# Performance work log

Measured on AMD Instinct MI355X. Metric: run time of the kernel, lower is better.

Reference implementation:

```python
import jax, jax.numpy as jnp
import numpy as np

A_MAX = 7  # 2**A_bits - 1 with A_bits=3
W_HI = 7   # torch.randint(0, 2**W_bits - 1) -> values in [0, 6]


def _conv_valid(x, w):
    # x: [N,C,H,W] float32, w: [O,I,kh,kw] float32; stride 1, no padding
    return jax.lax.conv_general_dilated(
        x, w, window_strides=(1, 1), padding='VALID',
        dimension_numbers=('NCHW', 'OIHW', 'NCHW'))


def setup_inputs() -> dict:
    key = jax.random.key(0)
    k_x, k_w = jax.random.split(key)
    x = jax.random.randint(k_x, (16, 64, 112, 112), 0, 8, dtype=jnp.int32)
    # 3-bit weights of the original 7x7 conv, values 0..6
    W7 = jax.random.randint(k_w, (128, 64, 7, 7), 0, W_HI).astype(jnp.float32)
    w1 = W7[:, :, :, 0:3]
    w2 = W7[:, :, :, 2:5]
    w2 = w2.at[:, :, :, 0].set(0.0)
    w2 = w2.at[:, :, :, 2].set(0.0)
    w3 = W7[:, :, :, 4:7]
    return {"x": x, "w1": w1, "w2": w2, "w3": w3}


def reference(x, w1, w2, w3):
    # 3-bit activation quantization: clip int input to [0, 7]
    xc = jnp.clip(x, 0, A_MAX).astype(jnp.float32)
    out1 = _conv_valid(xc[:, :, :, :-2], w1)   # [N,O,H-6,W-4]
    out2 = _conv_valid(xc, w2)                 # [N,O,H-6,W-2]
    out3 = _conv_valid(xc[:, :, :, 2:], w3)    # [N,O,H-6,W-4]
    # combine slices -> equivalent to valid 7x7 conv: [N,O,H-6,W-6]
    return out1[:, :, :, :-2] + out2[:, :, :, 2:-2] + out3[:, :, :, 2:]
```

## Files before the change

### kernel.cpp

```cpp
#include <hip/hip_runtime.h>
#include <cstdint>

typedef __attribute__((ext_vector_type(4))) int i32x4;

#define XROWS  22
#define ROWB   2048
#define WSLICE 8192
#define WB_BYTES 409600
#define XT_BYTES ((size_t)16 * 112 * 128 * 64)
#define GRID_MAIN 1536

__device__ __forceinline__ void g2lds16(const void* g, void* l) {
  __builtin_amdgcn_global_load_lds(
      (const __attribute__((address_space(1))) unsigned int*)g,
      (__attribute__((address_space(3))) unsigned int*)l, 16, 0, 0);
}

__global__ void prep_w(const float* __restrict__ w1,
                       const float* __restrict__ w2,
                       const float* __restrict__ w3,
                       signed char* __restrict__ wb) {
  int t = blockIdx.x * 256 + threadIdx.x;
  int lo = t & 15;
  int co = (t >> 4) & 127;
  int g  = (t >> 11) & 3;
  int s  = t >> 13;
  if (s >= 49) return;
  int kh = s / 7, kw = s % 7;
  int ci = g * 16 + lo;
  int base = ((co * 64 + ci) * 7 + kh) * 3;
  float v;
  if (kw < 3)       v = w1[base + kw];
  else if (kw == 3) v = w2[base + 1];
  else              v = w3[base + kw - 4];
  wb[t] = (signed char)(int)v;
}

__global__ void prep_xw(const int* __restrict__ x,
                        const float* __restrict__ w1,
                        const float* __restrict__ w2,
                        const float* __restrict__ w3,
                        signed char* __restrict__ xt,
                        signed char* __restrict__ wb) {
  __shared__ unsigned char T[64 * 68];
  const int tid = threadIdx.x;
  const int wt = blockIdx.x * 64, h = blockIdx.y, n = blockIdx.z;
  const int fid = (blockIdx.z * 112 + blockIdx.y) * 2 + blockIdx.x;

  if (fid < 1568) {
    int t = fid * 256 + tid;
    int lo = t & 15;
    int co = (t >> 4) & 127;
    int g  = (t >> 11) & 3;
    int s  = t >> 13;
    int kh = s / 7, kw = s % 7;
    int ci = g * 16 + lo;
    int base = ((co * 64 + ci) * 7 + kh) * 3;
    float v;
    if (kw < 3)       v = w1[base + kw];
    else if (kw == 3) v = w2[base + 1];
    else              v = w3[base + kw - 4];
    wb[t] = (signed char)(int)v;
  }

  {
    const int wr = tid & 63;
    const int cb = (tid >> 6) * 16;
    int ws = wt + wr; ws = ws < 112 ? ws : 111;
    const int* xp = x + (((size_t)n * 64 + cb) * 112 + h) * 112 + ws;
    #pragma unroll
    for (int g4 = 0; g4 < 4; ++g4) {
      uint32_t v = 0;
      #pragma unroll
      for (int j = 0; j < 4; ++j) {
        int a = xp[(g4 * 4 + j) * 12544];
        a = a < 0 ? 0 : (a > 7 ? 7 : a);
        v |= (uint32_t)a << (8 * j);
      }
      *(uint32_t*)&T[wr * 68 + cb + g4 * 4] = v;
    }
  }
  __syncthreads();
  {
    const int wo = tid >> 2, q = tid & 3;
    const int key = ((wt + wo) >> 1) & 3;
    const int sg = (q ^ key) << 4;
    int4 v;
    v.x = *(const int*)&T[wo * 68 + sg + 0];
    v.y = *(const int*)&T[wo * 68 + sg + 4];
    v.z = *(const int*)&T[wo * 68 + sg + 8];
    v.w = *(const int*)&T[wo * 68 + sg + 12];
    *(int4*)&xt[(((size_t)n * 112 + h) * 128 + wt + wo) * 64 + q * 16] = v;
  }
}

#define MFMA16(acc, a, b) acc = __builtin_amdgcn_mfma_i32_16x16x64_i8(a, b, acc, 0, 0, 0)

template<int PHASE>
__device__ __forceinline__ void kw_body(const int kw,
    const signed char* __restrict__ aB, const unsigned char* Xs,
    const int lrow, const int lkg,
    i32x4& A0, i32x4& A1, i32x4& A2, i32x4 (&acc)[16]) {
  const int w_l  = lrow + kw;
  const int bcol = w_l * 64 + ((lkg ^ ((w_l >> 1) & 3)) << 4);
  i32x4 B[16];
  #pragma unroll
  for (int b = 0; b < 16; ++b)
    B[b] = *(const i32x4*)&Xs[b * ROWB + bcol];

  #pragma unroll
  for (int kh = 0; kh < 7; ++kh) {
    const int nkh = (kh <= 3) ? kh + 3 : kh - 4;
    const int nkw = (kh <= 3) ? kw : (kw == 6 ? 0 : kw + 1);
    const signed char* apn = aB + (size_t)(nkh * 7 + nkw) * WSLICE;
    __builtin_amdgcn_s_setprio(1);
    if (((kh + PHASE) % 3) == 0) {
      MFMA16(acc[0], A0, B[kh]);
      if (kh < 6) B[kh] = *(const i32x4*)&Xs[(kh + 16) * ROWB + bcol];
      #pragma unroll
      for (int j = 1; j < 16; ++j) MFMA16(acc[j], A0, B[(kh + j) & 15]);
      __builtin_amdgcn_s_setprio(0);
      A0 = *(const i32x4*)apn;
    } else if (((kh + PHASE) % 3) == 1) {
      MFMA16(acc[0], A1, B[kh]);
      if (kh < 6) B[kh] = *(const i32x4*)&Xs[(kh + 16) * ROWB + bcol];
      #pragma unroll
      for (int j = 1; j < 16; ++j) MFMA16(acc[j], A1, B[(kh + j) & 15]);
      __builtin_amdgcn_s_setprio(0);
      A1 = *(const i32x4*)apn;
    } else {
      MFMA16(acc[0], A2, B[kh]);
      if (kh < 6) B[kh] = *(const i32x4*)&Xs[(kh + 16) * ROWB + bcol];
      #pragma unroll
      for (int j = 1; j < 16; ++j) MFMA16(acc[j], A2, B[(kh + j) & 15]);
      __builtin_amdgcn_s_setprio(0);
      A2 = *(const i32x4*)apn;
    }
  }
}

__global__ __launch_bounds__(256, 3)
void conv7s(const signed char* __restrict__ xt,
            const signed char* __restrict__ wb,
            float* __restrict__ out) {
  __shared__ __align__(16) unsigned char Xs[XROWS * ROWB];

  const int tid  = threadIdx.x;
  const int lane = tid & 63;
  const int wid  = tid >> 6;
  const int lrow = lane & 15;
  const int lkg  = lane >> 4;

  const int L  = blockIdx.x;
  const int Lp = (L & 7) * 192 + (L >> 3);
  const int npass = (L < 32) ? 2 : 1;

  const int k0 = (L >> 3) % 7;
  const int k1 = (k0 + 1) % 7;
  const int k2 = (k0 + 2) % 7;
  const int k3 = (k0 + 3) % 7;
  const int k4 = (k0 + 4) % 7;
  const int k5 = (k0 + 5) % 7;
  const int k6 = (k0 + 6) % 7;

  for (int pass = 0; pass < npass; ++pass) {
    const int t = (pass == 0) ? Lp : (GRID_MAIN + L);
    const int coh = t & 1;
    const int r2  = t >> 1;
    const int bx  = r2 % 7;
    const int t7  = r2 / 7;
    const int by  = t7 % 7;
    const int n   = t7 / 7;
    const int ho_base = by * 16;
    const int wo_base = bx * 16;

    const signed char* aB = wb + lkg * 2048 + (coh * 64 + wid * 16 + lrow) * 16;

    i32x4 A0 = *(const i32x4*)(aB + (size_t)(0 * 7 + k0) * WSLICE);
    i32x4 A1 = *(const i32x4*)(aB + (size_t)(1 * 7 + k0) * WSLICE);
    i32x4 A2 = *(const i32x4*)(aB + (size_t)(2 * 7 + k0) * WSLICE);

    if (pass) __syncthreads();

    for (int r = wid; r < XROWS; r += 4) {
      int h = ho_base + r; h = h < 112 ? h : 111;
      const signed char* src = xt + (((size_t)n * 112 + h) * 128 + wo_base) * 64;
      g2lds16(src + lane * 16, &Xs[r * ROWB]);
      g2lds16(src + 1024 + lane * 16, &Xs[r * ROWB + 1024]);
    }
    asm volatile("s_waitcnt vmcnt(0)" ::: "memory");
    __syncthreads();

    i32x4 acc[16];
    #pragma unroll
    for (int j = 0; j < 16; ++j) acc[j] = (i32x4){0, 0, 0, 0};

    kw_body<0>(k0, aB, Xs, lrow, lkg, A0, A1, A2, acc);
    kw_body<1>(k1, aB, Xs, lrow, lkg, A0, A1, A2, acc);
    kw_body<2>(k2, aB, Xs, lrow, lkg, A0, A1, A2, acc);
    kw_body<0>(k3, aB, Xs, lrow, lkg, A0, A1, A2, acc);
    kw_body<1>(k4, aB, Xs, lrow, lkg, A0, A1, A2, acc);
    kw_body<2>(k5, aB, Xs, lrow, lkg, A0, A1, A2, acc);
    kw_body<0>(k6, aB, Xs, lrow, lkg, A0, A1, A2, acc);

    const int wo = wo_base + lrow;
    if (wo < 106) {
      const int co = coh * 64 + wid * 16 + lkg * 4;
      #pragma unroll
      for (int j = 0; j < 16; ++j) {
        const int ho = ho_base + j;
        if (ho < 106) {
          float* op = out + (((size_t)n * 128 + co) * 106 + ho) * 106 + wo;
          #pragma unroll
          for (int jj = 0; jj < 4; ++jj)
            op[(size_t)jj * 11236] = (float)acc[j][jj];
        }
      }
    }
  }
}

__global__ __launch_bounds__(256, 3)
void conv7f(const int* __restrict__ x,
            const signed char* __restrict__ wb, float* __restrict__ out) {
  __shared__ __align__(16) unsigned char Xs[XROWS * ROWB];

  const int tid  = threadIdx.x;
  const int lane = tid & 63;
  const int wid  = tid >> 6;
  const int lrow = lane & 15;
  const int lkg  = lane >> 4;

  const int L  = blockIdx.x;
  const int Lp = (L & 7) * 196 + (L >> 3);
  const int coh = Lp & 1;
  const int r2  = Lp >> 1;
  const int bx  = r2 % 7;
  const int t7  = r2 / 7;
  const int by  = t7 % 7;
  const int n   = t7 / 7;
  const int ho_base = by * 16;
  const int wo_base = bx * 16;

  const signed char* aB = wb + lkg * 2048 + coh * 1024 + lrow * 16;
  i32x4 A[4];
  #pragma unroll
  for (int m = 0; m < 4; ++m) A[m] = *(const i32x4*)(aB + m * 256);

  {
    const int w_a  = tid & 15,       cg_a  = tid >> 4;
    const int w_b2 = 16 + (tid & 7), cg_b2 = tid >> 3;
    const bool doB = (tid < 128) && ((tid & 7) < 6);
    const int keyA = ((w_a >> 1) & 3) << 2;
    const int keyB = ((w_b2 >> 1) & 3) << 2;
    for (int r = 0; r < XROWS; ++r) {
      int h = ho_base + r; h = h < 112 ? h : 111;
      const int* xr = x + (size_t)n * 64 * 12544 + h * 112;
      {
        int wc = wo_base + w_a; wc = wc < 112 ? wc : 111;
        uint32_t v = 0;
        #pragma unroll
        for (int j = 0; j < 4; ++j) {
          int a = xr[(cg_a * 4 + j) * 12544 + wc];
          a = a < 0 ? 0 : (a > 7 ? 7 : a);
          v |= (uint32_t)a << (8 * j);
        }
        *(uint32_t*)&Xs[r * ROWB + w_a * 64 + ((cg_a ^ keyA) << 2)] = v;
      }
      if (doB) {
        int wc = wo_base + w_b2; wc = wc < 112 ? wc : 111;
        uint32_t v = 0;
        #pragma unroll
        for (int j = 0; j < 4; ++j) {
          int a = xr[(cg_b2 * 4 + j) * 12544 + wc];
          a = a < 0 ? 0 : (a > 7 ? 7 : a);
          v |= (uint32_t)a << (8 * j);
        }
        *(uint32_t*)&Xs[r * ROWB + w_b2 * 64 + ((cg_b2 ^ keyB) << 2)] = v;
      }
    }
  }
  __syncthreads();

  i32x4 acc[4][4];
  #pragma unroll
  for (int m = 0; m < 4; ++m)
    #pragma unroll
    for (int b = 0; b < 4; ++b)
      acc[m][b] = (i32x4){0, 0, 0, 0};

  const int rowB = wid * 4;

  for (int kw = 0; kw < 7; ++kw) {
    const int w_l  = lrow + kw;
    const int bcol = w_l * 64 + ((lkg ^ ((w_l >> 1) & 3)) << 4);
    i32x4 B[8];
    #pragma unroll
    for (int b = 0; b < 4; ++b)
      B[b] = *(const i32x4*)&Xs[(rowB + b) * ROWB + bcol];
    #pragma unroll
    for (int kh = 0; kh < 7; ++kh) {
      if (kh < 6)
        B[(kh + 4) & 7] = *(const i32x4*)&Xs[(rowB + kh + 4) * ROWB + bcol];
      const signed char* apn = aB + (size_t)(kh < 6 ? (kh + 1) * 7 + kw : kw + 1) * WSLICE;
      #pragma unroll
      for (int m = 0; m < 4; ++m) {
        #pragma unroll
        for (int b = 0; b < 4; ++b)
          MFMA16(acc[m][b], A[m], B[(kh + b) & 7]);
        A[m] = *(const i32x4*)(apn + m * 256);
      }
    }
  }

  const int wo = wo_base + lrow;
  if (wo < 106) {
    #pragma unroll
    for (int m = 0; m < 4; ++m) {
      const int co = coh * 64 + m * 16 + lkg * 4;
      #pragma unroll
      for (int b = 0; b < 4; ++b) {
        const int ho = ho_base + rowB + b;
        if (ho < 106) {
          float* op = out + (((size_t)n * 128 + co) * 106 + ho) * 106 + wo;
          #pragma unroll
          for (int j = 0; j < 4; ++j)
            op[(size_t)j * 11236] = (float)acc[m][b][j];
        }
      }
    }
  }
}

extern "C" void kernel_launch(void* const* d_in, const int* in_sizes, int n_in,
                              void* d_out, int out_size, void* d_ws, size_t ws_size,
                              hipStream_t stream) {
  const int*   x  = (const int*)d_in[0];
  const float* w1 = (const float*)d_in[1];
  const float* w2 = (const float*)d_in[2];
  const float* w3 = (const float*)d_in[3];
  float* outp = (float*)d_out;
  signed char* wbp = (signed char*)d_ws;
  signed char* xtp = wbp + WB_BYTES;

  if (ws_size >= WB_BYTES + XT_BYTES) {
    prep_xw<<<dim3(2, 112, 16), dim3(256), 0, stream>>>(x, w1, w2, w3, xtp, wbp);
    conv7s<<<dim3(GRID_MAIN), dim3(256), 0, stream>>>(xtp, wbp, outp);
  } else {
    prep_w<<<dim3(1568), dim3(256), 0, stream>>>(w1, w2, w3, wbp);
    conv7f<<<dim3(1568), dim3(256), 0, stream>>>(x, wbp, outp);
  }
}
```

Measured before the change: 68.48 us.

## Swap MFMA operands for vectorized stores and split tail tiles across four blocks

Swaps the A/B operands of the int8 MFMA so each lane holds four consecutive output width positions for a single channel. This allows 8-byte vector stores along the output row instead of four scalar stores strided by a channel plane. The 32 leftover tail tiles, previously done as a second full pass by 32 blocks, are now split into four height quarters over 128 blocks using a smaller kw_body variant. That shortens the critical path of the straggler blocks, at the cost of reloading some halo rows and weights for each quarter.

Result: no change. 69.59 us (+1.6%).

```diff
diff --git a/kernel.cpp b/kernel.cpp
--- a/kernel.cpp
+++ b/kernel.cpp
@@ -1,7 +1,8 @@
 #include <hip/hip_runtime.h>
 #include <cstdint>
 
-typedef __attribute__((ext_vector_type(4))) int i32x4;
+typedef __attribute__((ext_vector_type(4))) int   i32x4;
+typedef __attribute__((ext_vector_type(2))) float f32x2;
 
 #define XROWS  22
 #define ROWB   2048
@@ -94,7 +95,8 @@
   }
 }
 
-#define MFMA16(acc, a, b) acc = __builtin_amdgcn_mfma_i32_16x16x64_i8(a, b, acc, 0, 0, 0)
+#define MFMAX(acc, xf, wf) acc = __builtin_amdgcn_mfma_i32_16x16x64_i8(xf, wf, acc, 0, 0, 0)
+#define MFMA16(acc, a, b)  acc = __builtin_amdgcn_mfma_i32_16x16x64_i8(a, b, acc, 0, 0, 0)
 
 template<int PHASE>
 __device__ __forceinline__ void kw_body(const int kw,
@@ -115,25 +117,57 @@
     const signed char* apn = aB + (size_t)(nkh * 7 + nkw) * WSLICE;
     __builtin_amdgcn_s_setprio(1);
     if (((kh + PHASE) % 3) == 0) {
-      MFMA16(acc[0], A0, B[kh]);
+      MFMAX(acc[0], B[kh], A0);
       if (kh < 6) B[kh] = *(const i32x4*)&Xs[(kh + 16) * ROWB + bcol];
       #pragma unroll
-      for (int j = 1; j < 16; ++j) MFMA16(acc[j], A0, B[(kh + j) & 15]);
+      for (int j = 1; j < 16; ++j) MFMAX(acc[j], B[(kh + j) & 15], A0);
       __builtin_amdgcn_s_setprio(0);
       A0 = *(const i32x4*)apn;
     } else if (((kh + PHASE) % 3) == 1) {
-      MFMA16(acc[0], A1, B[kh]);
+      MFMAX(acc[0], B[kh], A1);
       if (kh < 6) B[kh] = *(const i32x4*)&Xs[(kh + 16) * ROWB + bcol];
       #pragma unroll
-      for (int j = 1; j < 16; ++j) MFMA16(acc[j], A1, B[(kh + j) & 15]);
+      for (int j = 1; j < 16; ++j) MFMAX(acc[j], B[(kh + j) & 15], A1);
       __builtin_amdgcn_s_setprio(0);
       A1 = *(const i32x4*)apn;
     } else {
-      MFMA16(acc[0], A2, B[kh]);
+      MFMAX(acc[0], B[kh], A2);
       if (kh < 6) B[kh] = *(const i32x4*)&Xs[(kh + 16) * ROWB + bcol];
       #pragma unroll
-      for (int j = 1; j < 16; ++j) MFMA16(acc[j], A2, B[(kh + j) & 15]);
+      for (int j = 1; j < 16; ++j) MFMAX(acc[j], B[(kh + j) & 15], A2);
       __builtin_amdgcn_s_setprio(0);
+      A2 = *(const i32x4*)apn;
+    }
+  }
+}
+
+template<int PHASE>
+__device__ __forceinline__ void kw_body_q(const int kw,
+    const signed char* __restrict__ aB, const unsigned char* Xs,
+    const int lrow, const int lkg,
+    i32x4& A0, i32x4& A1, i32x4& A2, i32x4 (&acc)[4]) {
+  const int w_l  = lrow + kw;
+  const int bcol = w_l * 64 + ((lkg ^ ((w_l >> 1) & 3)) << 4);
+  i32x4 B[10];
+  #pragma unroll
+  for (int b = 0; b < 10; ++b)
+    B[b] = *(const i32x4*)&Xs[b * ROWB + bcol];
+  #pragma unroll
+  for (int kh = 0; kh < 7; ++kh) {
+    const int nkh = (kh <= 3) ? kh + 3 : kh - 4;
+    const int nkw = (kh <= 3) ? kw : (kw == 6 ? 0 : kw + 1);
+    const signed char* apn = aB + (size_t)(nkh * 7 + nkw) * WSLICE;
+    if (((kh + PHASE) % 3) == 0) {
+      #pragma unroll
+      for (int j = 0; j < 4; ++j) MFMAX(acc[j], B[kh + j], A0);
+      A0 = *(const i32x4*)apn;
+    } else if (((kh + PHASE) % 3) == 1) {
+      #pragma unroll
+      for (int j = 0; j < 4; ++j) MFMAX(acc[j], B[kh + j], A1);
+      A1 = *(const i32x4*)apn;
+    } else {
+      #pragma unroll
+      for (int j = 0; j < 4; ++j) MFMAX(acc[j], B[kh + j], A2);
       A2 = *(const i32x4*)apn;
     }
   }
@@ -153,7 +187,6 @@
 
   const int L  = blockIdx.x;
   const int Lp = (L & 7) * 192 + (L >> 3);
-  const int npass = (L < 32) ? 2 : 1;
 
   const int k0 = (L >> 3) % 7;
   const int k1 = (k0 + 1) % 7;
@@ -163,8 +196,8 @@
   const int k5 = (k0 + 5) % 7;
   const int k6 = (k0 + 6) % 7;
 
-  for (int pass = 0; pass < npass; ++pass) {
-    const int t = (pass == 0) ? Lp : (GRID_MAIN + L);
+  {
+    const int t = Lp;
     const int coh = t & 1;
     const int r2  = t >> 1;
     const int bx  = r2 % 7;
@@ -180,8 +213,6 @@
     i32x4 A1 = *(const i32x4*)(aB + (size_t)(1 * 7 + k0) * WSLICE);
     i32x4 A2 = *(const i32x4*)(aB + (size_t)(2 * 7 + k0) * WSLICE);
 
-    if (pass) __syncthreads();
-
     for (int r = wid; r < XROWS; r += 4) {
       int h = ho_base + r; h = h < 112 ? h : 111;
       const signed char* src = xt + (((size_t)n * 112 + h) * 128 + wo_base) * 64;
@@ -203,17 +234,81 @@
     kw_body<2>(k5, aB, Xs, lrow, lkg, A0, A1, A2, acc);
     kw_body<0>(k6, aB, Xs, lrow, lkg, A0, A1, A2, acc);
 
-    const int wo = wo_base + lrow;
-    if (wo < 106) {
-      const int co = coh * 64 + wid * 16 + lkg * 4;
-      #pragma unroll
-      for (int j = 0; j < 16; ++j) {
-        const int ho = ho_base + j;
-        if (ho < 106) {
-          float* op = out + (((size_t)n * 128 + co) * 106 + ho) * 106 + wo;
+    const int co  = coh * 64 + wid * 16 + lrow;
+    const int wo0 = wo_base + lkg * 4;
+    const bool full4 = (wo0 + 3) < 106;
+    #pragma unroll
+    for (int j = 0; j < 16; ++j) {
+      const int ho = ho_base + j;
+      if (ho < 106) {
+        float* op = out + (((size_t)n * 128 + co) * 106 + ho) * 106 + wo0;
+        if (full4) {
+          *(f32x2*)(op)     = (f32x2){(float)acc[j][0], (float)acc[j][1]};
+          *(f32x2*)(op + 2) = (f32x2){(float)acc[j][2], (float)acc[j][3]};
+        } else {
           #pragma unroll
           for (int jj = 0; jj < 4; ++jj)
-            op[(size_t)jj * 11236] = (float)acc[j][jj];
+            if (wo0 + jj < 106) op[jj] = (float)acc[j][jj];
+        }
+      }
+    }
+  }
+
+  if (L < 128) {
+    const int t = GRID_MAIN + (L >> 2);
+    const int q = L & 3;
+    const int coh = t & 1;
+    const int r2  = t >> 1;
+    const int bx  = r2 % 7;
+    const int t7  = r2 / 7;
+    const int by  = t7 % 7;
+    const int n   = t7 / 7;
+    const int hob2    = by * 16 + q * 4;
+    const int wo_base = bx * 16;
+
+    const signed char* aB = wb + lkg * 2048 + (coh * 64 + wid * 16 + lrow) * 16;
+
+    __syncthreads();
+    for (int r = wid; r < 10; r += 4) {
+      int h = hob2 + r; h = h < 112 ? h : 111;
+      const signed char* src = xt + (((size_t)n * 112 + h) * 128 + wo_base) * 64;
+      g2lds16(src + lane * 16, &Xs[r * ROWB]);
+      g2lds16(src + 1024 + lane * 16, &Xs[r * ROWB + 1024]);
+    }
+    asm volatile("s_waitcnt vmcnt(0)" ::: "memory");
+    __syncthreads();
+
+    i32x4 acc[4];
+    #pragma unroll
+    for (int j = 0; j < 4; ++j) acc[j] = (i32x4){0, 0, 0, 0};
+
+    i32x4 A0 = *(const i32x4*)(aB);
+    i32x4 A1 = *(const i32x4*)(aB + (size_t)7 * WSLICE);
+    i32x4 A2 = *(const i32x4*)(aB + (size_t)14 * WSLICE);
+
+    kw_body_q<0>(0, aB, Xs, lrow, lkg, A0, A1, A2, acc);
+    kw_body_q<1>(1, aB, Xs, lrow, lkg, A0, A1, A2, acc);
+    kw_body_q<2>(2, aB, Xs, lrow, lkg, A0, A1, A2, acc);
+    kw_body_q<0>(3, aB, Xs, lrow, lkg, A0, A1, A2, acc);
+    kw_body_q<1>(4, aB, Xs, lrow, lkg, A0, A1, A2, acc);
+    kw_body_q<2>(5, aB, Xs, lrow, lkg, A0, A1, A2, acc);
+    kw_body_q<0>(6, aB, Xs, lrow, lkg, A0, A1, A2, acc);
+
+    const int co  = coh * 64 + wid * 16 + lrow;
+    const int wo0 = wo_base + lkg * 4;
+    const bool full4 = (wo0 + 3) < 106;
+    #pragma unroll
+    for (int j = 0; j < 4; ++j) {
+      const int ho = hob2 + j;
+      if (ho < 106) {
+        float* op = out + (((size_t)n * 128 + co) * 106 + ho) * 106 + wo0;
+        if (full4) {
+          *(f32x2*)(op)     = (f32x2){(float)acc[j][0], (float)acc[j][1]};
+          *(f32x2*)(op + 2) = (f32x2){(float)acc[j][2], (float)acc[j][3]};
+        } else {
+          #pragma unroll
+          for (int jj = 0; jj < 4; ++jj)
+            if (wo0 + jj < 106) op[jj] = (float)acc[j][jj];
         }
       }
     }
```
